# Performance work log

Hardware: AMD Instinct MI355X
Metric: run time of the kernel (lower is better)

Reference implementation:

```python
import jax, jax.numpy as jnp
import numpy as np
import math

HIDDEN = 1024
HEADS = 16
HEAD_DIM = HIDDEN // HEADS
B, S = 4, 2048


def setup_inputs() -> dict:
    key = jax.random.key(0)
    ks = jax.random.split(key, 9)
    std = 1.0 / math.sqrt(HIDDEN)
    return {
        "query": jax.random.normal(ks[0], (B, S, HIDDEN), jnp.float32),
        "key": jax.random.normal(ks[1], (B, S, HIDDEN), jnp.float32),
        "value": jax.random.normal(ks[2], (B, S, HIDDEN), jnp.float32),
        "q_w": jax.random.normal(ks[3], (HIDDEN, HIDDEN), jnp.float32) * std,
        "q_b": jax.random.normal(ks[4], (HIDDEN,), jnp.float32) * 0.02,
        "k_w": jax.random.normal(ks[5], (HIDDEN, HIDDEN), jnp.float32) * std,
        "k_b": jax.random.normal(ks[6], (HIDDEN,), jnp.float32) * 0.02,
        "v_w": jax.random.normal(ks[7], (HIDDEN, HIDDEN), jnp.float32) * std,
        "v_b": jax.random.normal(ks[8], (HIDDEN,), jnp.float32) * 0.02,
    }


def _split_heads(x):
    # [B, S, H] -> [B, heads, S, head_dim]
    b, s, _ = x.shape
    return x.reshape(b, s, HEADS, HEAD_DIM).transpose(0, 2, 1, 3)


def reference(query, key, value, q_w, q_b, k_w, k_b, v_w, v_b):
    # Linear projections (torch Linear: x @ W^T + b; here weights stored as [in, out])
    q = _split_heads(query @ q_w + q_b)   # [B, h, S, d]
    k = _split_heads(key @ k_w + k_b)
    v = _split_heads(value @ v_w + v_b)
    scale = 1.0 / math.sqrt(HEAD_DIM)
    scores = jnp.einsum("bhqd,bhkd->bhqk", q, k) * scale  # [B, h, S, S]
    # NOTE: faithful to source bug — context uses raw scaled scores, NOT softmax probs.
    # (softmax is computed in the original but its result is unused for the output.)
    ctx = jnp.einsum("bhqk,bhkd->bhqd", scores, v)
    ctx = ctx.transpose(0, 2, 1, 3).reshape(query.shape[0], query.shape[1], HIDDEN)
    return ctx
```

## Files before the change

### kernel.cpp

```cpp
#include <hip/hip_runtime.h>
#include <stdint.h>

#define HIDDEN 1024
#define HEADS 16
#define HEAD_DIM 64
#define BATCH 4
#define SEQ 2048
#define ROWS (BATCH * SEQ)

typedef float f32x4 __attribute__((ext_vector_type(4)));
typedef short bf16x8 __attribute__((ext_vector_type(8)));

__device__ __forceinline__ uint16_t f32_to_bf16_rne(float f) {
    uint32_t u = __float_as_uint(f);
    uint32_t r = u + 0x7FFFu + ((u >> 16) & 1u);
    return (uint16_t)(r >> 16);
}
__device__ __forceinline__ float bf16_to_f32(uint16_t u) {
    return __uint_as_float(((uint32_t)u) << 16);
}

__global__ __launch_bounds__(256) void cvt_kernel(const float* __restrict__ Xq,
                                                  const float* __restrict__ Xk,
                                                  const float* __restrict__ Xv,
                                                  uint16_t* __restrict__ Xb) {
    int z = blockIdx.x >> 12;
    const float* X = z == 0 ? Xq : (z == 1 ? Xk : Xv);
    uint16_t* out = Xb + (size_t)z * ROWS * HIDDEN;
    size_t e = ((size_t)(blockIdx.x & 4095) * 256 + threadIdx.x) * 8;
    float4 f0 = *(const float4*)(X + e);
    float4 f1 = *(const float4*)(X + e + 4);
    uint4 pk;
    pk.x = (uint32_t)f32_to_bf16_rne(f0.x) | ((uint32_t)f32_to_bf16_rne(f0.y) << 16);
    pk.y = (uint32_t)f32_to_bf16_rne(f0.z) | ((uint32_t)f32_to_bf16_rne(f0.w) << 16);
    pk.z = (uint32_t)f32_to_bf16_rne(f1.x) | ((uint32_t)f32_to_bf16_rne(f1.y) << 16);
    pk.w = (uint32_t)f32_to_bf16_rne(f1.z) | ((uint32_t)f32_to_bf16_rne(f1.w) << 16);
    *(uint4*)(out + e) = pk;
}

__global__ __launch_bounds__(256) void wt_kernel(const float* __restrict__ Wq,
                                                 const float* __restrict__ Wk,
                                                 const float* __restrict__ Wv,
                                                 uint16_t* __restrict__ Wt) {
    const float* W = blockIdx.z == 0 ? Wq : (blockIdx.z == 1 ? Wk : Wv);
    uint16_t* out = Wt + (size_t)blockIdx.z * HIDDEN * HIDDEN;
    __shared__ float tile[64][65];
    int k0 = blockIdx.x * 64, n0 = blockIdx.y * 64;
    int r = threadIdx.x >> 6, c = threadIdx.x & 63;
    for (int it = 0; it < 16; ++it) {
        int rr = r + 4 * it;
        tile[rr][c] = W[(size_t)(k0 + rr) * HIDDEN + n0 + c];
    }
    __syncthreads();
    for (int it = 0; it < 16; ++it) {
        int rr = r + 4 * it;
        out[(size_t)(n0 + rr) * HIDDEN + k0 + c] = f32_to_bf16_rne(tile[c][rr]);
    }
}

__global__ __launch_bounds__(256) void zero_kernel(float4* __restrict__ p) {
    int i = blockIdx.x * 256 + threadIdx.x;
    p[i] = make_float4(0.f, 0.f, 0.f, 0.f);
}

__global__ __launch_bounds__(256) void proj_gemm(const uint16_t* __restrict__ Xb,
                                                 const uint16_t* __restrict__ Wt,
                                                 const float* __restrict__ Bq,
                                                 const float* __restrict__ Bk,
                                                 const float* __restrict__ Bv,
                                                 uint16_t* __restrict__ QKV) {
    const int z = blockIdx.z;
    const uint16_t* X = Xb + (size_t)z * ROWS * HIDDEN;
    const uint16_t* W = Wt + (size_t)z * HIDDEN * HIDDEN;
    const float* bias = z == 0 ? Bq : (z == 1 ? Bk : Bv);
    uint16_t* out = QKV + (size_t)z * ROWS * HIDDEN;

    __shared__ uint16_t lds[16384];

    const int tid = threadIdx.x;
    const int lane = tid & 63;
    const int w = tid >> 6;
    const int wm = (w >> 1) * 64;
    const int wn = (w & 1) * 64;
    const int m_lane = lane & 15;
    const int kq = lane >> 4;
    const int m0 = blockIdx.x * 128;
    const int n0 = blockIdx.y * 128;

    f32x4 acc[4][4] = {};

    for (int kb = 0; kb < HIDDEN; kb += 64) {
        for (int t = 0; t < 4; ++t) {
            int gbase = (w * 4 + t) * 64;
            int g = gbase + lane;
            int r = g >> 3;
            int c = (g & 7) ^ (r & 7);
            const uint16_t* srcA = X + (size_t)(m0 + r) * HIDDEN + kb + c * 8;
            __builtin_amdgcn_global_load_lds(
                (const __attribute__((address_space(1))) uint32_t*)srcA,
                (__attribute__((address_space(3))) uint32_t*)(&lds[gbase * 8]),
                16, 0, 0);
            const uint16_t* srcB = W + (size_t)(n0 + r) * HIDDEN + kb + c * 8;
            __builtin_amdgcn_global_load_lds(
                (const __attribute__((address_space(1))) uint32_t*)srcB,
                (__attribute__((address_space(3))) uint32_t*)(&lds[8192 + gbase * 8]),
                16, 0, 0);
        }
        __syncthreads();
        for (int ks = 0; ks < 2; ++ks) {
            int cbase = ks * 4 + kq;
            bf16x8 af[4], bfr[4];
            for (int i = 0; i < 4; ++i) {
                int r = wm + i * 16 + m_lane;
                int p = cbase ^ (r & 7);
                af[i] = *(const bf16x8*)(&lds[r * 64 + p * 8]);
            }
            for (int j = 0; j < 4; ++j) {
                int nr = wn + j * 16 + m_lane;
                int p = cbase ^ (nr & 7);
                bfr[j] = *(const bf16x8*)(&lds[8192 + nr * 64 + p * 8]);
            }
            for (int i = 0; i < 4; ++i)
                for (int j = 0; j < 4; ++j)
                    acc[i][j] = __builtin_amdgcn_mfma_f32_16x16x32_bf16(
                        af[i], bfr[j], acc[i][j], 0, 0, 0);
        }
        __syncthreads();
    }

    for (int j = 0; j < 4; ++j) {
        int col = n0 + wn + j * 16 + m_lane;
        float bj = bias[col];
        for (int i = 0; i < 4; ++i) {
            int rbase = m0 + wm + i * 16 + kq * 4;
            for (int rg = 0; rg < 4; ++rg) {
                float v = acc[i][j][rg] + bj;
                out[(size_t)(rbase + rg) * HIDDEN + col] = f32_to_bf16_rne(v);
            }
        }
    }
}

__global__ __launch_bounds__(256) void kv_kernel(const uint16_t* __restrict__ K,
                                                 const uint16_t* __restrict__ V,
                                                 float* __restrict__ M) {
    const int bh = blockIdx.x;
    const int sc = blockIdx.y;
    const int b = bh >> 4, h = bh & 15;
    const int tid = threadIdx.x;
    const size_t base = ((size_t)b * SEQ + sc * 128) * HIDDEN + h * 64;

    __shared__ float kk[16][64];
    __shared__ float vv[16][64];
    float acc[4][4] = {};
    const int i0 = (tid >> 4) * 4, j0 = (tid & 15) * 4;

    for (int batch = 0; batch < 8; ++batch) {
        __syncthreads();
        {
            int t = tid & 127;
            int row = t >> 3, c = t & 7;
            const uint16_t* src =
                (tid < 128 ? K : V) + base + (size_t)(batch * 16 + row) * HIDDEN + c * 8;
            float* dst = (tid < 128 ? &kk[row][c * 8] : &vv[row][c * 8]);
            bf16x8 d = *(const bf16x8*)src;
            for (int e = 0; e < 8; ++e) dst[e] = bf16_to_f32((uint16_t)d[e]);
        }
        __syncthreads();
        for (int r = 0; r < 16; ++r) {
            f32x4 ka = *(const f32x4*)(&kk[r][i0]);
            f32x4 va = *(const f32x4*)(&vv[r][j0]);
            for (int a = 0; a < 4; ++a)
                for (int bb = 0; bb < 4; ++bb)
                    acc[a][bb] += ka[a] * va[bb];
        }
    }
    float* Mh = M + (size_t)bh * 4096;
    for (int a = 0; a < 4; ++a)
        for (int bb = 0; bb < 4; ++bb)
            atomicAdd(&Mh[(i0 + a) * 64 + j0 + bb], acc[a][bb] * 0.125f);
}

__global__ __launch_bounds__(256) void ctx_kernel(const uint16_t* __restrict__ Q,
                                                  const float* __restrict__ M,
                                                  float* __restrict__ out) {
    const int bh = blockIdx.x;
    const int sc = blockIdx.y;
    const int b = bh >> 4, h = bh & 15;
    const int tid = threadIdx.x;

    __shared__ float Mh[64][64];
    {
        const f32x4* Ms = (const f32x4*)(M + (size_t)bh * 4096);
        f32x4* Md = (f32x4*)Mh;
        for (int t = 0; t < 4; ++t) Md[t * 256 + tid] = Ms[t * 256 + tid];
    }
    __syncthreads();

    const int r0 = (tid >> 4) * 4;
    const int j0 = (tid & 15) * 4;
    const size_t row0 = (size_t)b * SEQ + sc * 64 + r0;
    const size_t qbase = row0 * HIDDEN + h * 64;

    f32x4 acc[4] = {};
    for (int ic = 0; ic < 8; ++ic) {
        bf16x8 qv[4];
        for (int rr = 0; rr < 4; ++rr)
            qv[rr] = *(const bf16x8*)(Q + qbase + (size_t)rr * HIDDEN + ic * 8);
        for (int e = 0; e < 8; ++e) {
            f32x4 m4 = *(const f32x4*)(&Mh[ic * 8 + e][j0]);
            for (int rr = 0; rr < 4; ++rr) {
                float q = bf16_to_f32((uint16_t)qv[rr][e]);
                acc[rr] += q * m4;
            }
        }
    }
    for (int rr = 0; rr < 4; ++rr)
        *(f32x4*)(out + (row0 + rr) * HIDDEN + h * 64 + j0) = acc[rr];
}

extern "C" void kernel_launch(void* const* d_in, const int* in_sizes, int n_in,
                              void* d_out, int out_size, void* d_ws, size_t ws_size,
                              hipStream_t stream) {
    const float* Xq = (const float*)d_in[0];
    const float* Xk = (const float*)d_in[1];
    const float* Xv = (const float*)d_in[2];
    const float* Wq = (const float*)d_in[3];
    const float* Bq = (const float*)d_in[4];
    const float* Wk = (const float*)d_in[5];
    const float* Bk = (const float*)d_in[6];
    const float* Wv = (const float*)d_in[7];
    const float* Bv = (const float*)d_in[8];
    float* out = (float*)d_out;

    char* ws = (char*)d_ws;
    uint16_t* Wt = (uint16_t*)ws;
    uint16_t* Xb = (uint16_t*)(ws + 6291456);
    uint16_t* QKV = (uint16_t*)(ws + 6291456 + 50331648);
    float* M = (float*)(ws + 6291456 + 2 * 50331648ll);

    cvt_kernel<<<dim3(3 * 4096), 256, 0, stream>>>(Xq, Xk, Xv, Xb);
    wt_kernel<<<dim3(16, 16, 3), 256, 0, stream>>>(Wq, Wk, Wv, Wt);
    zero_kernel<<<dim3(256), 256, 0, stream>>>((float4*)M);
    proj_gemm<<<dim3(64, 8, 3), 256, 0, stream>>>(Xb, Wt, Bq, Bk, Bv, QKV);

    const uint16_t* Qp = QKV;
    const uint16_t* Kp = QKV + (size_t)ROWS * HIDDEN;
    const uint16_t* Vp = QKV + 2 * (size_t)ROWS * HIDDEN;
    kv_kernel<<<dim3(64, 16), 256, 0, stream>>>(Kp, Vp, M);
    ctx_kernel<<<dim3(64, 32), 256, 0, stream>>>(Qp, M, out);
}
```

Measured before the change: 311.4 us.

## Fold K^T V into Q projection weights per batch, skipping Q materialization

Because the context is linear in Q, ctx = X_q (W_q M) + b_q M, where M = K^T V/8 per head. A small kernel now forms per-batch, block-diagonal-by-head folded weights W_q·M and bias b_q·M. A single MFMA GEMM then computes the output straight from bf16 X_q, replacing the Q projection GEMM, the Q write and read, and the separate ctx kernel. Zeroing M is merged into the convert kernel. This adds a per-batch 1024x1024 weight build and one more bf16 rounding of W_q·M.

```diff
diff --git a/kernel.cpp b/kernel.cpp
--- a/kernel.cpp
+++ b/kernel.cpp
@@ -23,7 +23,10 @@
 __global__ __launch_bounds__(256) void cvt_kernel(const float* __restrict__ Xq,
                                                   const float* __restrict__ Xk,
                                                   const float* __restrict__ Xv,
-                                                  uint16_t* __restrict__ Xb) {
+                                                  uint16_t* __restrict__ Xb,
+                                                  float4* __restrict__ M) {
+    if (blockIdx.x < 256)
+        M[blockIdx.x * 256 + threadIdx.x] = make_float4(0.f, 0.f, 0.f, 0.f);
     int z = blockIdx.x >> 12;
     const float* X = z == 0 ? Xq : (z == 1 ? Xk : Xv);
     uint16_t* out = Xb + (size_t)z * ROWS * HIDDEN;
@@ -38,11 +41,10 @@
     *(uint4*)(out + e) = pk;
 }
 
-__global__ __launch_bounds__(256) void wt_kernel(const float* __restrict__ Wq,
-                                                 const float* __restrict__ Wk,
+__global__ __launch_bounds__(256) void wt_kernel(const float* __restrict__ Wk,
                                                  const float* __restrict__ Wv,
                                                  uint16_t* __restrict__ Wt) {
-    const float* W = blockIdx.z == 0 ? Wq : (blockIdx.z == 1 ? Wk : Wv);
+    const float* W = blockIdx.z == 0 ? Wk : Wv;
     uint16_t* out = Wt + (size_t)blockIdx.z * HIDDEN * HIDDEN;
     __shared__ float tile[64][65];
     int k0 = blockIdx.x * 64, n0 = blockIdx.y * 64;
@@ -58,22 +60,16 @@
     }
 }
 
-__global__ __launch_bounds__(256) void zero_kernel(float4* __restrict__ p) {
-    int i = blockIdx.x * 256 + threadIdx.x;
-    p[i] = make_float4(0.f, 0.f, 0.f, 0.f);
-}
-
-__global__ __launch_bounds__(256) void proj_gemm(const uint16_t* __restrict__ Xb,
+__global__ __launch_bounds__(256) void proj_gemm(const uint16_t* __restrict__ Xkv,
                                                  const uint16_t* __restrict__ Wt,
-                                                 const float* __restrict__ Bq,
                                                  const float* __restrict__ Bk,
                                                  const float* __restrict__ Bv,
-                                                 uint16_t* __restrict__ QKV) {
+                                                 uint16_t* __restrict__ KV) {
     const int z = blockIdx.z;
-    const uint16_t* X = Xb + (size_t)z * ROWS * HIDDEN;
+    const uint16_t* X = Xkv + (size_t)z * ROWS * HIDDEN;
     const uint16_t* W = Wt + (size_t)z * HIDDEN * HIDDEN;
-    const float* bias = z == 0 ? Bq : (z == 1 ? Bk : Bv);
-    uint16_t* out = QKV + (size_t)z * ROWS * HIDDEN;
+    const float* bias = z == 0 ? Bk : Bv;
+    uint16_t* out = KV + (size_t)z * ROWS * HIDDEN;
 
     __shared__ uint16_t lds[16384];
 
@@ -141,9 +137,10 @@
     }
 }
 
-__global__ __launch_bounds__(256) void kv_kernel(const uint16_t* __restrict__ K,
-                                                 const uint16_t* __restrict__ V,
+__global__ __launch_bounds__(256) void kv_kernel(const uint16_t* __restrict__ KV,
                                                  float* __restrict__ M) {
+    const uint16_t* K = KV;
+    const uint16_t* V = KV + (size_t)ROWS * HIDDEN;
     const int bh = blockIdx.x;
     const int sc = blockIdx.y;
     const int b = bh >> 4, h = bh & 15;
@@ -181,42 +178,117 @@
             atomicAdd(&Mh[(i0 + a) * 64 + j0 + bb], acc[a][bb] * 0.125f);
 }
 
-__global__ __launch_bounds__(256) void ctx_kernel(const uint16_t* __restrict__ Q,
-                                                  const float* __restrict__ M,
+__global__ __launch_bounds__(256) void wprime_kernel(const float* __restrict__ Wq,
+                                                     const float* __restrict__ bq,
+                                                     const float* __restrict__ M,
+                                                     uint16_t* __restrict__ Wpt,
+                                                     float* __restrict__ bp) {
+    const int h = blockIdx.x;
+    const int r0 = blockIdx.y * 64;
+    const int b = blockIdx.z;
+    const int tid = threadIdx.x;
+
+    __shared__ float Mh[64][65];
+    __shared__ float Wl[64][65];
+    for (int it = 0; it < 16; ++it) {
+        int e = it * 256 + tid;
+        int a = e >> 6, c = e & 63;
+        Mh[a][c] = M[((size_t)(b * 16 + h)) * 4096 + e];
+        Wl[a][c] = Wq[(size_t)(r0 + a) * HIDDEN + h * 64 + c];
+    }
+    __syncthreads();
+
+    const int r = tid & 63;
+    const int jbase = tid >> 6;
+    float acc[16] = {};
+    for (int i = 0; i < 64; ++i) {
+        float wv = Wl[r][i];
+        for (int jj = 0; jj < 16; ++jj)
+            acc[jj] += wv * Mh[i][jbase + 4 * jj];
+    }
+    uint16_t* Wb = Wpt + (size_t)b * HIDDEN * HIDDEN;
+    for (int jj = 0; jj < 16; ++jj) {
+        int n = h * 64 + jbase + 4 * jj;
+        Wb[(size_t)n * HIDDEN + r0 + r] = f32_to_bf16_rne(acc[jj]);
+    }
+
+    if (blockIdx.y == 0 && tid < 64) {
+        int j = tid;
+        float s = 0.f;
+        for (int i = 0; i < 64; ++i) s += bq[h * 64 + i] * Mh[i][j];
+        bp[b * HIDDEN + h * 64 + j] = s;
+    }
+}
+
+__global__ __launch_bounds__(256) void final_gemm(const uint16_t* __restrict__ Xq,
+                                                  const uint16_t* __restrict__ Wpt,
+                                                  const float* __restrict__ bp,
                                                   float* __restrict__ out) {
-    const int bh = blockIdx.x;
-    const int sc = blockIdx.y;
-    const int b = bh >> 4, h = bh & 15;
+    __shared__ uint16_t lds[16384];
+
     const int tid = threadIdx.x;
-
-    __shared__ float Mh[64][64];
-    {
-        const f32x4* Ms = (const f32x4*)(M + (size_t)bh * 4096);
-        f32x4* Md = (f32x4*)Mh;
-        for (int t = 0; t < 4; ++t) Md[t * 256 + tid] = Ms[t * 256 + tid];
-    }
-    __syncthreads();
-
-    const int r0 = (tid >> 4) * 4;
-    const int j0 = (tid & 15) * 4;
-    const size_t row0 = (size_t)b * SEQ + sc * 64 + r0;
-    const size_t qbase = row0 * HIDDEN + h * 64;
-
-    f32x4 acc[4] = {};
-    for (int ic = 0; ic < 8; ++ic) {
-        bf16x8 qv[4];
-        for (int rr = 0; rr < 4; ++rr)
-            qv[rr] = *(const bf16x8*)(Q + qbase + (size_t)rr * HIDDEN + ic * 8);
-        for (int e = 0; e < 8; ++e) {
-            f32x4 m4 = *(const f32x4*)(&Mh[ic * 8 + e][j0]);
-            for (int rr = 0; rr < 4; ++rr) {
-                float q = bf16_to_f32((uint16_t)qv[rr][e]);
-                acc[rr] += q * m4;
-            }
-        }
-    }
-    for (int rr = 0; rr < 4; ++rr)
-        *(f32x4*)(out + (row0 + rr) * HIDDEN + h * 64 + j0) = acc[rr];
+    const int lane = tid & 63;
+    const int w = tid >> 6;
+    const int wm = (w >> 1) * 64;
+    const int wn = (w & 1) * 64;
+    const int m_lane = lane & 15;
+    const int kq = lane >> 4;
+    const int m0 = blockIdx.x * 128;
+    const int n0 = blockIdx.y * 128;
+    const int batch = m0 >> 11;
+    const uint16_t* W = Wpt + (size_t)batch * HIDDEN * HIDDEN;
+    const float* bias = bp + batch * HIDDEN;
+
+    f32x4 acc[4][4] = {};
+
+    for (int kb = 0; kb < HIDDEN; kb += 64) {
+        for (int t = 0; t < 4; ++t) {
+            int gbase = (w * 4 + t) * 64;
+            int g = gbase + lane;
+            int r = g >> 3;
+            int c = (g & 7) ^ (r & 7);
+            const uint16_t* srcA = Xq + (size_t)(m0 + r) * HIDDEN + kb + c * 8;
+            __builtin_amdgcn_global_load_lds(
+                (const __attribute__((address_space(1))) uint32_t*)srcA,
+                (__attribute__((address_space(3))) uint32_t*)(&lds[gbase * 8]),
+                16, 0, 0);
+            const uint16_t* srcB = W + (size_t)(n0 + r) * HIDDEN + kb + c * 8;
+            __builtin_amdgcn_global_load_lds(
+                (const __attribute__((address_space(1))) uint32_t*)srcB,
+                (__attribute__((address_space(3))) uint32_t*)(&lds[8192 + gbase * 8]),
+                16, 0, 0);
+        }
+        __syncthreads();
+        for (int ks = 0; ks < 2; ++ks) {
+            int cbase = ks * 4 + kq;
+            bf16x8 af[4], bfr[4];
+            for (int i = 0; i < 4; ++i) {
+                int r = wm + i * 16 + m_lane;
+                int p = cbase ^ (r & 7);
+                af[i] = *(const bf16x8*)(&lds[r * 64 + p * 8]);
+            }
+            for (int j = 0; j < 4; ++j) {
+                int nr = wn + j * 16 + m_lane;
+                int p = cbase ^ (nr & 7);
+                bfr[j] = *(const bf16x8*)(&lds[8192 + nr * 64 + p * 8]);
+            }
+            for (int i = 0; i < 4; ++i)
+                for (int j = 0; j < 4; ++j)
+                    acc[i][j] = __builtin_amdgcn_mfma_f32_16x16x32_bf16(
+                        af[i], bfr[j], acc[i][j], 0, 0, 0);
+        }
+        __syncthreads();
+    }
+
+    for (int j = 0; j < 4; ++j) {
+        int col = n0 + wn + j * 16 + m_lane;
+        float bj = bias[col];
+        for (int i = 0; i < 4; ++i) {
+            int rbase = m0 + wm + i * 16 + kq * 4;
+            for (int rg = 0; rg < 4; ++rg)
+                out[(size_t)(rbase + rg) * HIDDEN + col] = acc[i][j][rg] + bj;
+        }
+    }
 }
 
 extern "C" void kernel_launch(void* const* d_in, const int* in_sizes, int n_in,
@@ -234,19 +306,19 @@
     float* out = (float*)d_out;
 
     char* ws = (char*)d_ws;
-    uint16_t* Wt = (uint16_t*)ws;
-    uint16_t* Xb = (uint16_t*)(ws + 6291456);
-    uint16_t* QKV = (uint16_t*)(ws + 6291456 + 50331648);
-    float* M = (float*)(ws + 6291456 + 2 * 50331648ll);
-
-    cvt_kernel<<<dim3(3 * 4096), 256, 0, stream>>>(Xq, Xk, Xv, Xb);
-    wt_kernel<<<dim3(16, 16, 3), 256, 0, stream>>>(Wq, Wk, Wv, Wt);
-    zero_kernel<<<dim3(256), 256, 0, stream>>>((float4*)M);
-    proj_gemm<<<dim3(64, 8, 3), 256, 0, stream>>>(Xb, Wt, Bq, Bk, Bv, QKV);
-
-    const uint16_t* Qp = QKV;
-    const uint16_t* Kp = QKV + (size_t)ROWS * HIDDEN;
-    const uint16_t* Vp = QKV + 2 * (size_t)ROWS * HIDDEN;
-    kv_kernel<<<dim3(64, 16), 256, 0, stream>>>(Kp, Vp, M);
-    ctx_kernel<<<dim3(64, 32), 256, 0, stream>>>(Qp, M, out);
-}
+    uint16_t* Xb = (uint16_t*)ws;
+    uint16_t* KV = (uint16_t*)(ws + 50331648);
+    uint16_t* Wt = (uint16_t*)(ws + 83886080);
+    float* M = (float*)(ws + 88080384);
+    uint16_t* Wpt = (uint16_t*)(ws + 89128960);
+    float* bp = (float*)(ws + 97517568);
+
+    cvt_kernel<<<dim3(3 * 4096), 256, 0, stream>>>(Xq, Xk, Xv, Xb, (float4*)M);
+    wt_kernel<<<dim3(16, 16, 2), 256, 0, stream>>>(Wk, Wv, Wt);
+
+    const uint16_t* Xkv = Xb + (size_t)ROWS * HIDDEN;
+    proj_gemm<<<dim3(64, 8, 2), 256, 0, stream>>>(Xkv, Wt, Bk, Bv, KV);
+    kv_kernel<<<dim3(64, 16), 256, 0, stream>>>(KV, M);
+    wprime_kernel<<<dim3(16, 16, 4), 256, 0, stream>>>(Wq, Bq, M, Wpt, bp);
+    final_gemm<<<dim3(64, 8), 256, 0, stream>>>(Xb, Wpt, bp, out);
+}
```

Result: no change. 310.4 us (-0.3%).
